# Kernel optimization log

Measured on AMD Instinct MI355X. Metric: run time of the kernel, lower is better.

The kernel has to match this reference:

```python
import jax, jax.numpy as jnp
import numpy as np

B, N_IN, N_HID, T = 64, 512, 512, 512


def setup_inputs() -> dict:
    key = jax.random.key(0)
    k1, k2, k3, k4, k5 = jax.random.split(key, 5)
    scale = 1.0 / np.sqrt(N_HID).astype(np.float32)
    return {
        "X": jax.random.normal(k1, (B, N_IN, T), dtype=jnp.float32),
        "Wax": jax.random.normal(k2, (N_IN, N_HID), dtype=jnp.float32) * scale,
        "Waa": jax.random.normal(k3, (N_HID, N_HID), dtype=jnp.float32) * scale,
        "bx": jax.random.normal(k4, (N_HID,), dtype=jnp.float32) * scale,
        "ba": jax.random.normal(k5, (N_HID,), dtype=jnp.float32) * scale,
    }


def reference(X, Wax, Waa, bx, ba):
    # X: [B, n_in, T]. a_{t+1} = tanh(x_t @ Wax + bx + a_t @ Waa + ba)
    # Precompute the input projections for all timesteps in one big GEMM:
    # [T, B, n_hid]
    Xt = jnp.transpose(X, (2, 0, 1))  # [T, B, n_in]
    inp_proj = jnp.einsum('tbi,ih->tbh', Xt, Wax) + bx + ba

    def step(a, u):
        a_next = jnp.tanh(u + a @ Waa)
        return a_next, a_next

    a0 = jnp.zeros((X.shape[0], Waa.shape[0]), dtype=X.dtype)
    _, A = jax.lax.scan(step, a0, inp_proj)
    return A  # [T, B, n_hid] == stacked A[1:] of the torch module
```

## Files before the change

kernel.cpp:

```cpp
#include <hip/hip_runtime.h>
#include <math.h>

#define BB   64
#define NIN  512
#define NH   512
#define TT   512

typedef _Float16 half2_t __attribute__((ext_vector_type(2)));
typedef _Float16 half8_t __attribute__((ext_vector_type(8)));
typedef float    f32x4  __attribute__((ext_vector_type(4)));

__device__ __forceinline__ unsigned pk16(float x, float y) {
    unsigned lo = (unsigned)__builtin_bit_cast(unsigned short, (_Float16)x);
    unsigned hi = (unsigned)__builtin_bit_cast(unsigned short, (_Float16)y);
    return lo | (hi << 16);
}

__device__ __forceinline__ float tanh_fast(float x) {
    float ax = __builtin_fabsf(x);
    float e  = __builtin_amdgcn_exp2f(-2.885390082f * ax);
    float r  = (1.0f - e) * __builtin_amdgcn_rcpf(1.0f + e);
    return __builtin_copysignf(r, x);
}

#define NX4 (BB * (NIN / 2) * (TT / 4))
#define NW4 ((NIN / 2) * (NH / 4))

__global__ __launch_bounds__(256) void pack_f16(
    const float* __restrict__ X, const float* __restrict__ Wax,
    unsigned* __restrict__ Xp, unsigned* __restrict__ Wp)
{
    const int gid = blockIdx.x * 256 + threadIdx.x;
    if (gid < NX4) {
        const int t4 = gid & (TT / 4 - 1);
        const int pr = gid >> 7;
        const int j  = pr & (NIN / 2 - 1);
        const int b  = pr >> 8;
        float4 r0 = *(const float4*)&X[((size_t)b * NIN + 2 * j    ) * TT + t4 * 4];
        float4 r1 = *(const float4*)&X[((size_t)b * NIN + 2 * j + 1) * TT + t4 * 4];
        uint4 o;
        o.x = pk16(r0.x, r1.x); o.y = pk16(r0.y, r1.y);
        o.z = pk16(r0.z, r1.z); o.w = pk16(r0.w, r1.w);
        *(uint4*)&Xp[(size_t)pr * TT + t4 * 4] = o;
    } else {
        const int g = gid - NX4;
        if (g < NW4) {
            const int h4 = g & (NH / 4 - 1);
            const int j  = g >> 7;
            float4 r0 = *(const float4*)&Wax[((size_t)(2 * j    )) * NH + h4 * 4];
            float4 r1 = *(const float4*)&Wax[((size_t)(2 * j + 1)) * NH + h4 * 4];
            uint4 o;
            o.x = pk16(r0.x, r1.x); o.y = pk16(r0.y, r1.y);
            o.z = pk16(r0.z, r1.z); o.w = pk16(r0.w, r1.w);
            *(uint4*)&Wp[(size_t)j * NH + h4 * 4] = o;
        }
    }
}

__global__ __launch_bounds__(256) void inp_proj_mfma_pk(
    const unsigned* __restrict__ Xp, const unsigned* __restrict__ Wp,
    const float* __restrict__ bx, const float* __restrict__ ba,
    float* __restrict__ out)
{
    __shared__ unsigned Xsp[16][132];
    __shared__ unsigned Wsp[16][132];

    const int b   = blockIdx.z;
    const int t0  = blockIdx.y * 128;
    const int h0  = blockIdx.x * 128;
    const int tid = threadIdx.x;
    const int lane = tid & 63;
    const int wid  = tid >> 6;
    const int wm   = wid >> 1;
    const int wn   = wid & 1;
    const int q    = lane >> 4;
    const int r16  = lane & 15;

    const int lr = tid >> 4;
    const int lc = (tid & 15) * 8;

    const unsigned* Xb = Xp + (size_t)b * (NIN / 2) * TT;

    f32x4 acc[4][4] = {};

    for (int p0 = 0; p0 < NIN / 2; p0 += 16) {
        const unsigned* Arow = &Xb[(size_t)(p0 + lr) * TT + t0 + lc];
        const unsigned* Brow = &Wp[(size_t)(p0 + lr) * NH + h0 + lc];
        uint4 xa = *(const uint4*)&Arow[0];
        uint4 xb = *(const uint4*)&Arow[4];
        uint4 wa = *(const uint4*)&Brow[0];
        uint4 wb = *(const uint4*)&Brow[4];

        __syncthreads();
        *(uint4*)&Xsp[lr][lc]     = xa;
        *(uint4*)&Xsp[lr][lc + 4] = xb;
        *(uint4*)&Wsp[lr][lc]     = wa;
        *(uint4*)&Wsp[lr][lc + 4] = wb;
        __syncthreads();

        uint4 af[4], bf[4];
#pragma unroll
        for (int mt = 0; mt < 4; ++mt) {
            const int tc = wm * 64 + mt * 16 + r16;
            af[mt].x = Xsp[4 * q + 0][tc];
            af[mt].y = Xsp[4 * q + 1][tc];
            af[mt].z = Xsp[4 * q + 2][tc];
            af[mt].w = Xsp[4 * q + 3][tc];
        }
#pragma unroll
        for (int nt = 0; nt < 4; ++nt) {
            const int hc = wn * 64 + nt * 16 + r16;
            bf[nt].x = Wsp[4 * q + 0][hc];
            bf[nt].y = Wsp[4 * q + 1][hc];
            bf[nt].z = Wsp[4 * q + 2][hc];
            bf[nt].w = Wsp[4 * q + 3][hc];
        }
#pragma unroll
        for (int mt = 0; mt < 4; ++mt)
#pragma unroll
            for (int nt = 0; nt < 4; ++nt)
                acc[mt][nt] = __builtin_amdgcn_mfma_f32_16x16x32_f16(
                    __builtin_bit_cast(half8_t, af[mt]),
                    __builtin_bit_cast(half8_t, bf[nt]),
                    acc[mt][nt], 0, 0, 0);
    }

#pragma unroll
    for (int nt = 0; nt < 4; ++nt) {
        const int h = h0 + wn * 64 + nt * 16 + r16;
        const float bias = bx[h] + ba[h];
#pragma unroll
        for (int mt = 0; mt < 4; ++mt) {
            const int trow = t0 + wm * 64 + mt * 16 + q * 4;
#pragma unroll
            for (int rr = 0; rr < 4; ++rr) {
                out[(size_t)(trow + rr) * (BB * NH) + (size_t)b * NH + h] =
                    acc[mt][nt][rr] + bias;
            }
        }
    }
}

__global__ __launch_bounds__(256) void inp_proj_mfma(
    const float* __restrict__ X, const float* __restrict__ Wax,
    const float* __restrict__ bx, const float* __restrict__ ba,
    float* __restrict__ out)
{
    __shared__ unsigned Xsp[16][132];
    __shared__ unsigned Wsp[16][132];

    const int b   = blockIdx.z;
    const int t0  = blockIdx.y * 128;
    const int h0  = blockIdx.x * 128;
    const int tid = threadIdx.x;
    const int lane = tid & 63;
    const int wid  = tid >> 6;
    const int wm   = wid >> 1;
    const int wn   = wid & 1;
    const int q    = lane >> 4;
    const int r16  = lane & 15;

    const int lr = tid >> 4;
    const int lc = (tid & 15) * 8;

    const float* Xb = X + (size_t)b * NIN * TT;

    f32x4 acc[4][4] = {};

    for (int i0 = 0; i0 < NIN; i0 += 32) {
        const int k0 = i0 + 2 * lr, k1 = k0 + 1;
        float4 xa0 = *(const float4*)&Xb[(size_t)k0 * TT + t0 + lc];
        float4 xa1 = *(const float4*)&Xb[(size_t)k0 * TT + t0 + lc + 4];
        float4 xb0 = *(const float4*)&Xb[(size_t)k1 * TT + t0 + lc];
        float4 xb1 = *(const float4*)&Xb[(size_t)k1 * TT + t0 + lc + 4];
        float4 wa0 = *(const float4*)&Wax[(size_t)k0 * NH + h0 + lc];
        float4 wa1 = *(const float4*)&Wax[(size_t)k0 * NH + h0 + lc + 4];
        float4 wb0 = *(const float4*)&Wax[(size_t)k1 * NH + h0 + lc];
        float4 wb1 = *(const float4*)&Wax[(size_t)k1 * NH + h0 + lc + 4];

        uint4 xp0, xp1, wp0, wp1;
        xp0.x = pk16(xa0.x, xb0.x); xp0.y = pk16(xa0.y, xb0.y);
        xp0.z = pk16(xa0.z, xb0.z); xp0.w = pk16(xa0.w, xb0.w);
        xp1.x = pk16(xa1.x, xb1.x); xp1.y = pk16(xa1.y, xb1.y);
        xp1.z = pk16(xa1.z, xb1.z); xp1.w = pk16(xa1.w, xb1.w);
        wp0.x = pk16(wa0.x, wb0.x); wp0.y = pk16(wa0.y, wb0.y);
        wp0.z = pk16(wa0.z, wb0.z); wp0.w = pk16(wa0.w, wb0.w);
        wp1.x = pk16(wa1.x, wb1.x); wp1.y = pk16(wa1.y, wb1.y);
        wp1.z = pk16(wa1.z, wb1.z); wp1.w = pk16(wa1.w, wb1.w);

        __syncthreads();
        *(uint4*)&Xsp[lr][lc]     = xp0;
        *(uint4*)&Xsp[lr][lc + 4] = xp1;
        *(uint4*)&Wsp[lr][lc]     = wp0;
        *(uint4*)&Wsp[lr][lc + 4] = wp1;
        __syncthreads();

        uint4 af[4], bf[4];
#pragma unroll
        for (int mt = 0; mt < 4; ++mt) {
            const int tc = wm * 64 + mt * 16 + r16;
            af[mt].x = Xsp[4 * q + 0][tc];
            af[mt].y = Xsp[4 * q + 1][tc];
            af[mt].z = Xsp[4 * q + 2][tc];
            af[mt].w = Xsp[4 * q + 3][tc];
        }
#pragma unroll
        for (int nt = 0; nt < 4; ++nt) {
            const int hc = wn * 64 + nt * 16 + r16;
            bf[nt].x = Wsp[4 * q + 0][hc];
            bf[nt].y = Wsp[4 * q + 1][hc];
            bf[nt].z = Wsp[4 * q + 2][hc];
            bf[nt].w = Wsp[4 * q + 3][hc];
        }
#pragma unroll
        for (int mt = 0; mt < 4; ++mt)
#pragma unroll
            for (int nt = 0; nt < 4; ++nt)
                acc[mt][nt] = __builtin_amdgcn_mfma_f32_16x16x32_f16(
                    __builtin_bit_cast(half8_t, af[mt]),
                    __builtin_bit_cast(half8_t, bf[nt]),
                    acc[mt][nt], 0, 0, 0);
    }

#pragma unroll
    for (int nt = 0; nt < 4; ++nt) {
        const int h = h0 + wn * 64 + nt * 16 + r16;
        const float bias = bx[h] + ba[h];
#pragma unroll
        for (int mt = 0; mt < 4; ++mt) {
            const int trow = t0 + wm * 64 + mt * 16 + q * 4;
#pragma unroll
            for (int rr = 0; rr < 4; ++rr) {
                out[(size_t)(trow + rr) * (BB * NH) + (size_t)b * NH + h] =
                    acc[mt][nt][rr] + bias;
            }
        }
    }
}

#define RKT 12
#define LKT 4

__global__ __launch_bounds__(1024, 4) void rnn_scan_v9(
    const float* __restrict__ Waa, float* __restrict__ out)
{
    __shared__ uint4 wlds[LKT * 2][1024];
    __shared__ unsigned short a_h[2][NH];

    const int tid = threadIdx.x;
    const int b   = blockIdx.x;
    const int w   = tid >> 6;
    const int l   = tid & 63;
    const int q   = l >> 4;
    const int c0  = w * 32 + (l & 15);
    const int c1  = c0 + 16;

    uint4 br0[RKT], br1[RKT];
#pragma unroll
    for (int kk = 0; kk < RKT; ++kk) {
        const int kb = kk * 32 + 8 * q;
        uint4 v0, v1;
        v0.x = pk16(Waa[(size_t)(kb + 0) * NH + c0], Waa[(size_t)(kb + 1) * NH + c0]);
        v0.y = pk16(Waa[(size_t)(kb + 2) * NH + c0], Waa[(size_t)(kb + 3) * NH + c0]);
        v0.z = pk16(Waa[(size_t)(kb + 4) * NH + c0], Waa[(size_t)(kb + 5) * NH + c0]);
        v0.w = pk16(Waa[(size_t)(kb + 6) * NH + c0], Waa[(size_t)(kb + 7) * NH + c0]);
        v1.x = pk16(Waa[(size_t)(kb + 0) * NH + c1], Waa[(size_t)(kb + 1) * NH + c1]);
        v1.y = pk16(Waa[(size_t)(kb + 2) * NH + c1], Waa[(size_t)(kb + 3) * NH + c1]);
        v1.z = pk16(Waa[(size_t)(kb + 4) * NH + c1], Waa[(size_t)(kb + 5) * NH + c1]);
        v1.w = pk16(Waa[(size_t)(kb + 6) * NH + c1], Waa[(size_t)(kb + 7) * NH + c1]);
        br0[kk] = v0;
        br1[kk] = v1;
    }
#pragma unroll
    for (int kk = 0; kk < LKT; ++kk) {
        const int kb = (RKT + kk) * 32 + 8 * q;
        uint4 v0, v1;
        v0.x = pk16(Waa[(size_t)(kb + 0) * NH + c0], Waa[(size_t)(kb + 1) * NH + c0]);
        v0.y = pk16(Waa[(size_t)(kb + 2) * NH + c0], Waa[(size_t)(kb + 3) * NH + c0]);
        v0.z = pk16(Waa[(size_t)(kb + 4) * NH + c0], Waa[(size_t)(kb + 5) * NH + c0]);
        v0.w = pk16(Waa[(size_t)(kb + 6) * NH + c0], Waa[(size_t)(kb + 7) * NH + c0]);
        v1.x = pk16(Waa[(size_t)(kb + 0) * NH + c1], Waa[(size_t)(kb + 1) * NH + c1]);
        v1.y = pk16(Waa[(size_t)(kb + 2) * NH + c1], Waa[(size_t)(kb + 3) * NH + c1]);
        v1.z = pk16(Waa[(size_t)(kb + 4) * NH + c1], Waa[(size_t)(kb + 5) * NH + c1]);
        v1.w = pk16(Waa[(size_t)(kb + 6) * NH + c1], Waa[(size_t)(kb + 7) * NH + c1]);
        wlds[kk * 2 + 0][tid] = v0;
        wlds[kk * 2 + 1][tid] = v1;
    }

    if (tid < 256) *(unsigned*)&a_h[0][tid * 2] = 0u;
    __syncthreads();

    const float* ub0 = out + (size_t)b * NH + c0;
    const float* ub1 = out + (size_t)b * NH + c1;
    float u0 = ub0[0], u1 = ub1[0];

    for (int t = 0; t < TT; ++t) {
        const int tn = (t + 1 < TT) ? (t + 1) : (TT - 1);
        float un0 = ub0[(size_t)tn * (BB * NH)];
        float un1 = ub1[(size_t)tn * (BB * NH)];

        const unsigned short* ac = a_h[t & 1];
        f32x4 acc0 = {}, acc1 = {};
#pragma unroll
        for (int kk = 0; kk < 16; ++kk) {
            uint4 av = *(const uint4*)&ac[kk * 32 + q * 8];
            half8_t A = __builtin_bit_cast(half8_t, av);
            uint4 b0, b1;
            if (kk < RKT) {
                b0 = br0[kk];
                b1 = br1[kk];
            } else {
                b0 = wlds[(kk - RKT) * 2 + 0][tid];
                b1 = wlds[(kk - RKT) * 2 + 1][tid];
            }
            acc0 = __builtin_amdgcn_mfma_f32_16x16x32_f16(
                A, __builtin_bit_cast(half8_t, b0), acc0, 0, 0, 0);
            acc1 = __builtin_amdgcn_mfma_f32_16x16x32_f16(
                A, __builtin_bit_cast(half8_t, b1), acc1, 0, 0, 0);
        }

        float an0 = tanh_fast(u0 + acc0[0]);
        float an1 = tanh_fast(u1 + acc1[0]);

        unsigned short* an = a_h[(t + 1) & 1];
        if (l < 16) {
            an[c0] = __builtin_bit_cast(unsigned short, (_Float16)an0);
            an[c1] = __builtin_bit_cast(unsigned short, (_Float16)an1);
            out[(size_t)t * (BB * NH) + (size_t)b * NH + c0] = an0;
            out[(size_t)t * (BB * NH) + (size_t)b * NH + c1] = an1;
        }
        u0 = un0;
        u1 = un1;
        __builtin_amdgcn_s_waitcnt(0xC07F);
        __builtin_amdgcn_s_barrier();
    }
}

extern "C" void kernel_launch(void* const* d_in, const int* in_sizes, int n_in,
                              void* d_out, int out_size, void* d_ws, size_t ws_size,
                              hipStream_t stream) {
    const float* X   = (const float*)d_in[0];
    const float* Wax = (const float*)d_in[1];
    const float* Waa = (const float*)d_in[2];
    const float* bx  = (const float*)d_in[3];
    const float* ba  = (const float*)d_in[4];
    float* out = (float*)d_out;

    const size_t xp_dw = (size_t)BB * (NIN / 2) * TT;
    const size_t wp_dw = (size_t)(NIN / 2) * NH;
    const size_t need  = (xp_dw + wp_dw) * sizeof(unsigned);

    if (ws_size >= need) {
        unsigned* Xp = (unsigned*)d_ws;
        unsigned* Wp = Xp + xp_dw;
        const int npack = (NX4 + NW4 + 255) / 256;
        pack_f16<<<npack, 256, 0, stream>>>(X, Wax, Xp, Wp);
        dim3 g1(NH / 128, TT / 128, BB);
        inp_proj_mfma_pk<<<g1, 256, 0, stream>>>(Xp, Wp, bx, ba, out);
    } else {
        dim3 g1(NH / 128, TT / 128, BB);
        inp_proj_mfma<<<g1, 256, 0, stream>>>(X, Wax, bx, ba, out);
    }
    rnn_scan_v9<<<BB, 1024, 0, stream>>>(Waa, out);
}
```

Measured before the change: 920.9 us.

## Split recurrent step between MFMA waves and VALU dot2 waves with LDS reduction

The scan kernel now splits its 1024 threads into two halves. Half use the existing MFMA path for hidden columns 0-255. The other half compute columns 256-511 with packed fp16 dot2 instructions, broadcasting activations via readlane and reducing split-K partials through LDS. The aim is to use the vector ALUs alongside the matrix cores and lower register pressure per MFMA wave. The cost is an extra barrier and an LDS reduction on every timestep.

Measured after the change: 973.0 us. 1.06x slower.

```diff
diff --git a/kernel.cpp b/kernel.cpp
--- a/kernel.cpp
+++ b/kernel.cpp
@@ -14,6 +14,11 @@
     unsigned lo = (unsigned)__builtin_bit_cast(unsigned short, (_Float16)x);
     unsigned hi = (unsigned)__builtin_bit_cast(unsigned short, (_Float16)y);
     return lo | (hi << 16);
+}
+
+__device__ __forceinline__ float dot2u(unsigned w, unsigned a, float acc) {
+    return __builtin_amdgcn_fdot2(__builtin_bit_cast(half2_t, w),
+                                  __builtin_bit_cast(half2_t, a), acc, false);
 }
 
 __device__ __forceinline__ float tanh_fast(float x) {
@@ -240,99 +245,197 @@
 
 #define RKT 12
 #define LKT 4
-
-__global__ __launch_bounds__(1024, 4) void rnn_scan_v9(
+#define NRP 24
+#define NLP 8
+
+__device__ __forceinline__ unsigned bline(unsigned a, int l) {
+    return (unsigned)__builtin_amdgcn_readlane((int)a, l);
+}
+
+__global__ __launch_bounds__(1024, 4) void rnn_scan_v10(
     const float* __restrict__ Waa, float* __restrict__ out)
 {
-    __shared__ uint4 wlds[LKT * 2][1024];
+    __shared__ uint4    wldsA[LKT * 2][512];
+    __shared__ uint4    wlds2[NLP][512];
     __shared__ unsigned short a_h[2][NH];
+    __shared__ float    part[8][260];
 
     const int tid = threadIdx.x;
     const int b   = blockIdx.x;
-    const int w   = tid >> 6;
-    const int l   = tid & 63;
-    const int q   = l >> 4;
-    const int c0  = w * 32 + (l & 15);
-    const int c1  = c0 + 16;
-
-    uint4 br0[RKT], br1[RKT];
-#pragma unroll
-    for (int kk = 0; kk < RKT; ++kk) {
-        const int kb = kk * 32 + 8 * q;
-        uint4 v0, v1;
-        v0.x = pk16(Waa[(size_t)(kb + 0) * NH + c0], Waa[(size_t)(kb + 1) * NH + c0]);
-        v0.y = pk16(Waa[(size_t)(kb + 2) * NH + c0], Waa[(size_t)(kb + 3) * NH + c0]);
-        v0.z = pk16(Waa[(size_t)(kb + 4) * NH + c0], Waa[(size_t)(kb + 5) * NH + c0]);
-        v0.w = pk16(Waa[(size_t)(kb + 6) * NH + c0], Waa[(size_t)(kb + 7) * NH + c0]);
-        v1.x = pk16(Waa[(size_t)(kb + 0) * NH + c1], Waa[(size_t)(kb + 1) * NH + c1]);
-        v1.y = pk16(Waa[(size_t)(kb + 2) * NH + c1], Waa[(size_t)(kb + 3) * NH + c1]);
-        v1.z = pk16(Waa[(size_t)(kb + 4) * NH + c1], Waa[(size_t)(kb + 5) * NH + c1]);
-        v1.w = pk16(Waa[(size_t)(kb + 6) * NH + c1], Waa[(size_t)(kb + 7) * NH + c1]);
-        br0[kk] = v0;
-        br1[kk] = v1;
-    }
-#pragma unroll
-    for (int kk = 0; kk < LKT; ++kk) {
-        const int kb = (RKT + kk) * 32 + 8 * q;
-        uint4 v0, v1;
-        v0.x = pk16(Waa[(size_t)(kb + 0) * NH + c0], Waa[(size_t)(kb + 1) * NH + c0]);
-        v0.y = pk16(Waa[(size_t)(kb + 2) * NH + c0], Waa[(size_t)(kb + 3) * NH + c0]);
-        v0.z = pk16(Waa[(size_t)(kb + 4) * NH + c0], Waa[(size_t)(kb + 5) * NH + c0]);
-        v0.w = pk16(Waa[(size_t)(kb + 6) * NH + c0], Waa[(size_t)(kb + 7) * NH + c0]);
-        v1.x = pk16(Waa[(size_t)(kb + 0) * NH + c1], Waa[(size_t)(kb + 1) * NH + c1]);
-        v1.y = pk16(Waa[(size_t)(kb + 2) * NH + c1], Waa[(size_t)(kb + 3) * NH + c1]);
-        v1.z = pk16(Waa[(size_t)(kb + 4) * NH + c1], Waa[(size_t)(kb + 5) * NH + c1]);
-        v1.w = pk16(Waa[(size_t)(kb + 6) * NH + c1], Waa[(size_t)(kb + 7) * NH + c1]);
-        wlds[kk * 2 + 0][tid] = v0;
-        wlds[kk * 2 + 1][tid] = v1;
-    }
 
     if (tid < 256) *(unsigned*)&a_h[0][tid * 2] = 0u;
-    __syncthreads();
-
-    const float* ub0 = out + (size_t)b * NH + c0;
-    const float* ub1 = out + (size_t)b * NH + c1;
-    float u0 = ub0[0], u1 = ub1[0];
-
-    for (int t = 0; t < TT; ++t) {
-        const int tn = (t + 1 < TT) ? (t + 1) : (TT - 1);
-        float un0 = ub0[(size_t)tn * (BB * NH)];
-        float un1 = ub1[(size_t)tn * (BB * NH)];
-
-        const unsigned short* ac = a_h[t & 1];
-        f32x4 acc0 = {}, acc1 = {};
-#pragma unroll
-        for (int kk = 0; kk < 16; ++kk) {
-            uint4 av = *(const uint4*)&ac[kk * 32 + q * 8];
-            half8_t A = __builtin_bit_cast(half8_t, av);
-            uint4 b0, b1;
-            if (kk < RKT) {
-                b0 = br0[kk];
-                b1 = br1[kk];
-            } else {
-                b0 = wlds[(kk - RKT) * 2 + 0][tid];
-                b1 = wlds[(kk - RKT) * 2 + 1][tid];
-            }
-            acc0 = __builtin_amdgcn_mfma_f32_16x16x32_f16(
-                A, __builtin_bit_cast(half8_t, b0), acc0, 0, 0, 0);
-            acc1 = __builtin_amdgcn_mfma_f32_16x16x32_f16(
-                A, __builtin_bit_cast(half8_t, b1), acc1, 0, 0, 0);
-        }
-
-        float an0 = tanh_fast(u0 + acc0[0]);
-        float an1 = tanh_fast(u1 + acc1[0]);
-
-        unsigned short* an = a_h[(t + 1) & 1];
-        if (l < 16) {
-            an[c0] = __builtin_bit_cast(unsigned short, (_Float16)an0);
-            an[c1] = __builtin_bit_cast(unsigned short, (_Float16)an1);
-            out[(size_t)t * (BB * NH) + (size_t)b * NH + c0] = an0;
-            out[(size_t)t * (BB * NH) + (size_t)b * NH + c1] = an1;
-        }
-        u0 = un0;
-        u1 = un1;
-        __builtin_amdgcn_s_waitcnt(0xC07F);
-        __builtin_amdgcn_s_barrier();
+
+    if (tid < 512) {
+        const int w2 = tid >> 6;
+        const int l  = tid & 63;
+        const int q  = l >> 4;
+        const int c0 = w2 * 32 + (l & 15);
+        const int c1 = c0 + 16;
+
+        uint4 br0[RKT], br1[RKT];
+#pragma unroll
+        for (int kk = 0; kk < RKT; ++kk) {
+            const int kb = kk * 32 + 8 * q;
+            uint4 v0, v1;
+            v0.x = pk16(Waa[(size_t)(kb + 0) * NH + c0], Waa[(size_t)(kb + 1) * NH + c0]);
+            v0.y = pk16(Waa[(size_t)(kb + 2) * NH + c0], Waa[(size_t)(kb + 3) * NH + c0]);
+            v0.z = pk16(Waa[(size_t)(kb + 4) * NH + c0], Waa[(size_t)(kb + 5) * NH + c0]);
+            v0.w = pk16(Waa[(size_t)(kb + 6) * NH + c0], Waa[(size_t)(kb + 7) * NH + c0]);
+            v1.x = pk16(Waa[(size_t)(kb + 0) * NH + c1], Waa[(size_t)(kb + 1) * NH + c1]);
+            v1.y = pk16(Waa[(size_t)(kb + 2) * NH + c1], Waa[(size_t)(kb + 3) * NH + c1]);
+            v1.z = pk16(Waa[(size_t)(kb + 4) * NH + c1], Waa[(size_t)(kb + 5) * NH + c1]);
+            v1.w = pk16(Waa[(size_t)(kb + 6) * NH + c1], Waa[(size_t)(kb + 7) * NH + c1]);
+            br0[kk] = v0;
+            br1[kk] = v1;
+        }
+#pragma unroll
+        for (int kk = 0; kk < LKT; ++kk) {
+            const int kb = (RKT + kk) * 32 + 8 * q;
+            uint4 v0, v1;
+            v0.x = pk16(Waa[(size_t)(kb + 0) * NH + c0], Waa[(size_t)(kb + 1) * NH + c0]);
+            v0.y = pk16(Waa[(size_t)(kb + 2) * NH + c0], Waa[(size_t)(kb + 3) * NH + c0]);
+            v0.z = pk16(Waa[(size_t)(kb + 4) * NH + c0], Waa[(size_t)(kb + 5) * NH + c0]);
+            v0.w = pk16(Waa[(size_t)(kb + 6) * NH + c0], Waa[(size_t)(kb + 7) * NH + c0]);
+            v1.x = pk16(Waa[(size_t)(kb + 0) * NH + c1], Waa[(size_t)(kb + 1) * NH + c1]);
+            v1.y = pk16(Waa[(size_t)(kb + 2) * NH + c1], Waa[(size_t)(kb + 3) * NH + c1]);
+            v1.z = pk16(Waa[(size_t)(kb + 4) * NH + c1], Waa[(size_t)(kb + 5) * NH + c1]);
+            v1.w = pk16(Waa[(size_t)(kb + 6) * NH + c1], Waa[(size_t)(kb + 7) * NH + c1]);
+            wldsA[kk * 2 + 0][tid] = v0;
+            wldsA[kk * 2 + 1][tid] = v1;
+        }
+        __syncthreads();
+
+        const float* ub0 = out + (size_t)b * NH + c0;
+        const float* ub1 = out + (size_t)b * NH + c1;
+        float u0 = ub0[0], u1 = ub1[0];
+
+        for (int t = 0; t < TT; ++t) {
+            const int tn = (t + 1 < TT) ? (t + 1) : (TT - 1);
+            float un0 = ub0[(size_t)tn * (BB * NH)];
+            float un1 = ub1[(size_t)tn * (BB * NH)];
+
+            const unsigned short* ac = a_h[t & 1];
+            f32x4 acc0 = {}, acc1 = {};
+#pragma unroll
+            for (int kk = 0; kk < 16; ++kk) {
+                uint4 av = *(const uint4*)&ac[kk * 32 + q * 8];
+                half8_t A = __builtin_bit_cast(half8_t, av);
+                uint4 b0, b1;
+                if (kk < RKT) {
+                    b0 = br0[kk];
+                    b1 = br1[kk];
+                } else {
+                    b0 = wldsA[(kk - RKT) * 2 + 0][tid];
+                    b1 = wldsA[(kk - RKT) * 2 + 1][tid];
+                }
+                acc0 = __builtin_amdgcn_mfma_f32_16x16x32_f16(
+                    A, __builtin_bit_cast(half8_t, b0), acc0, 0, 0, 0);
+                acc1 = __builtin_amdgcn_mfma_f32_16x16x32_f16(
+                    A, __builtin_bit_cast(half8_t, b1), acc1, 0, 0, 0);
+            }
+
+            float an0 = tanh_fast(u0 + acc0[0]);
+            float an1 = tanh_fast(u1 + acc1[0]);
+
+            unsigned short* an = a_h[(t + 1) & 1];
+            if (l < 16) {
+                an[c0] = __builtin_bit_cast(unsigned short, (_Float16)an0);
+                an[c1] = __builtin_bit_cast(unsigned short, (_Float16)an1);
+                out[(size_t)t * (BB * NH) + (size_t)b * NH + c0] = an0;
+                out[(size_t)t * (BB * NH) + (size_t)b * NH + c1] = an1;
+            }
+            u0 = un0;
+            u1 = un1;
+            __builtin_amdgcn_s_waitcnt(0xC07F);
+            __builtin_amdgcn_s_barrier();
+            __builtin_amdgcn_s_barrier();
+        }
+    } else {
+        const int t2   = tid - 512;
+        const int kq   = t2 >> 6;
+        const int cidx = t2 & 63;
+        const int h4   = 256 + cidx * 4;
+        const int l32  = t2 & 31;
+
+        unsigned w0[NRP], w1[NRP], w2r[NRP], w3[NRP];
+#pragma unroll
+        for (int j = 0; j < NRP; ++j) {
+            const int k = kq * 64 + 2 * j;
+            float4 r0 = *(const float4*)&Waa[(size_t)k       * NH + h4];
+            float4 r1 = *(const float4*)&Waa[(size_t)(k + 1) * NH + h4];
+            w0[j]  = pk16(r0.x, r1.x);
+            w1[j]  = pk16(r0.y, r1.y);
+            w2r[j] = pk16(r0.z, r1.z);
+            w3[j]  = pk16(r0.w, r1.w);
+        }
+#pragma unroll
+        for (int p = 0; p < NLP; ++p) {
+            const int k = kq * 64 + 2 * (NRP + p);
+            float4 r0 = *(const float4*)&Waa[(size_t)k       * NH + h4];
+            float4 r1 = *(const float4*)&Waa[(size_t)(k + 1) * NH + h4];
+            uint4 wv;
+            wv.x = pk16(r0.x, r1.x);
+            wv.y = pk16(r0.y, r1.y);
+            wv.z = pk16(r0.z, r1.z);
+            wv.w = pk16(r0.w, r1.w);
+            wlds2[p][t2] = wv;
+        }
+        __syncthreads();
+
+        const bool red = (t2 < 256);
+        const int  hc  = 256 + (t2 & 255);
+        float* ob = out + (size_t)b * NH + hc;
+        float u_cur = red ? ob[0] : 0.0f;
+
+        for (int t = 0; t < TT; ++t) {
+            const int tn = (t + 1 < TT) ? (t + 1) : (TT - 1);
+            float u_next = red ? ob[(size_t)tn * (BB * NH)] : 0.0f;
+
+            unsigned a_loc = ((const unsigned*)a_h[t & 1])[kq * 32 + l32];
+
+            float acc0 = 0.f, acc1 = 0.f, acc2 = 0.f, acc3 = 0.f;
+#pragma unroll
+            for (int j = 0; j < NRP; j += 2) {
+                unsigned ra = bline(a_loc, j);
+                unsigned rb = bline(a_loc, j + 1);
+                acc0 = dot2u(w0[j],  ra, acc0);
+                acc1 = dot2u(w1[j],  ra, acc1);
+                acc2 = dot2u(w2r[j], ra, acc2);
+                acc3 = dot2u(w3[j],  ra, acc3);
+                acc0 = dot2u(w0[j + 1],  rb, acc0);
+                acc1 = dot2u(w1[j + 1],  rb, acc1);
+                acc2 = dot2u(w2r[j + 1], rb, acc2);
+                acc3 = dot2u(w3[j + 1],  rb, acc3);
+            }
+#pragma unroll
+            for (int p = 0; p < NLP; ++p) {
+                unsigned ra = bline(a_loc, NRP + p);
+                uint4 v = wlds2[p][t2];
+                acc0 = dot2u(v.x, ra, acc0);
+                acc1 = dot2u(v.y, ra, acc1);
+                acc2 = dot2u(v.z, ra, acc2);
+                acc3 = dot2u(v.w, ra, acc3);
+            }
+
+            float4 pv; pv.x = acc0; pv.y = acc1; pv.z = acc2; pv.w = acc3;
+            *(float4*)&part[kq][cidx * 4] = pv;
+            __builtin_amdgcn_s_waitcnt(0xC07F);
+            __builtin_amdgcn_s_barrier();
+
+            if (red) {
+                const int j = t2 & 255;
+                float x = u_cur +
+                    (((part[0][j] + part[1][j]) + (part[2][j] + part[3][j])) +
+                     ((part[4][j] + part[5][j]) + (part[6][j] + part[7][j])));
+                float an = tanh_fast(x);
+                ob[(size_t)t * (BB * NH)] = an;
+                a_h[(t + 1) & 1][hc] =
+                    __builtin_bit_cast(unsigned short, (_Float16)an);
+            }
+            u_cur = u_next;
+            __builtin_amdgcn_s_waitcnt(0xC07F);
+            __builtin_amdgcn_s_barrier();
+        }
     }
 }
 
@@ -361,5 +464,5 @@
         dim3 g1(NH / 128, TT / 128, BB);
         inp_proj_mfma<<<g1, 256, 0, stream>>>(X, Wax, bx, ba, out);
     }
-    rnn_scan_v9<<<BB, 1024, 0, stream>>>(Waa, out);
-}
+    rnn_scan_v10<<<BB, 1024, 0, stream>>>(Waa, out);
+}
```
